# Kernel tuning notes

Hardware: AMD Instinct MI355X
Metric: run time of the kernel (lower is better)

The kernel has to match this reference:

```python
import jax, jax.numpy as jnp
import numpy as np

VOCAB = 30001  # vocab_size + 1
EMB = 64
CHAR = 50
RNN = 128
TAGS = 9
B, T = 256, 512
D_IN = EMB + CHAR  # 114


def lstm_scan(x, Wx, Wh, b):
    # x: [T, B, D]; Keras LSTM gate order i, f, g(c), o; sigmoid/tanh activations.
    Bsz = x.shape[1]
    H = Wh.shape[0]
    def step(carry, xt):
        h, c = carry
        z = xt @ Wx + h @ Wh + b  # [B, 4H]
        i, f, g, o = jnp.split(z, 4, axis=-1)
        c = jax.nn.sigmoid(f) * c + jax.nn.sigmoid(i) * jnp.tanh(g)
        h = jax.nn.sigmoid(o) * jnp.tanh(c)
        return (h, c), h
    init = (jnp.zeros((Bsz, H), x.dtype), jnp.zeros((Bsz, H), x.dtype))
    _, hs = jax.lax.scan(step, init, x)
    return hs  # [T, B, H]


def crf_log_likelihood(logits, labels, lengths, trans):
    # logits: [B,T,K]; labels: [B,T] int; lengths: [B] int; trans: [K,K]
    Bsz, Tlen, K = logits.shape
    mask = (jnp.arange(Tlen)[None, :] < lengths[:, None]).astype(logits.dtype)  # [B,T]
    # gold path score: unary + pairwise transition terms
    unary = jnp.take_along_axis(logits, labels[..., None], axis=-1)[..., 0]  # [B,T]
    unary_score = jnp.sum(unary * mask, axis=1)
    binary = trans[labels[:, :-1], labels[:, 1:]]  # [B,T-1]
    binary_score = jnp.sum(binary * mask[:, 1:], axis=1)
    seq_score = unary_score + binary_score
    # forward algorithm (log-domain scan over time)
    logits_t = jnp.transpose(logits, (1, 0, 2))  # [T,B,K]
    mask_t = jnp.transpose(mask[:, 1:])          # [T-1,B]
    def step(alpha, inp):
        logit_t, m = inp
        new = jax.nn.logsumexp(alpha[:, :, None] + trans[None], axis=1) + logit_t
        alpha = jnp.where(m[:, None] > 0, new, alpha)
        return alpha, None
    alpha, _ = jax.lax.scan(step, logits_t[0], (logits_t[1:], mask_t))
    log_norm = jax.nn.logsumexp(alpha, axis=1)
    log_norm = jnp.where(lengths > 0, log_norm, jnp.zeros_like(log_norm))
    return seq_score - log_norm


def setup_inputs() -> dict:
    key = jax.random.key(0)
    ks = jax.random.split(key, 12)
    inputs = jax.random.randint(ks[0], (B, T), 0, 30000, dtype=jnp.int32)
    char_embeddings = jax.random.normal(ks[1], (B, T, CHAR), dtype=jnp.float32)
    labels = jax.random.randint(ks[2], (B, T), 0, TAGS, dtype=jnp.int32)
    E = 0.1 * jax.random.normal(ks[3], (VOCAB, EMB), dtype=jnp.float32)
    s_in = 1.0 / np.sqrt(D_IN)
    s_h = 1.0 / np.sqrt(RNN)
    Wx_f = s_in * jax.random.normal(ks[4], (D_IN, 4 * RNN), dtype=jnp.float32)
    Wh_f = s_h * jax.random.normal(ks[5], (RNN, 4 * RNN), dtype=jnp.float32)
    b_f = jnp.zeros((4 * RNN,), jnp.float32)
    Wx_b = s_in * jax.random.normal(ks[6], (D_IN, 4 * RNN), dtype=jnp.float32)
    Wh_b = s_h * jax.random.normal(ks[7], (RNN, 4 * RNN), dtype=jnp.float32)
    b_b = jnp.zeros((4 * RNN,), jnp.float32)
    Wd = (1.0 / np.sqrt(2 * RNN)) * jax.random.normal(ks[8], (2 * RNN, TAGS), dtype=jnp.float32)
    bd = jnp.zeros((TAGS,), jnp.float32)
    transition = jax.random.uniform(ks[9], (TAGS, TAGS), dtype=jnp.float32)
    return {"inputs": inputs, "char_embeddings": char_embeddings, "labels": labels,
            "E": E, "Wx_f": Wx_f, "Wh_f": Wh_f, "b_f": b_f,
            "Wx_b": Wx_b, "Wh_b": Wh_b, "b_b": b_b,
            "Wd": Wd, "bd": bd, "transition": transition}


def reference(inputs, char_embeddings, labels, E, Wx_f, Wh_f, b_f, Wx_b, Wh_b, b_b, Wd, bd, transition):
    emb = E[inputs]                                      # [B,T,64]
    x = jnp.concatenate([emb, char_embeddings], axis=2)  # [B,T,114]
    xt = jnp.transpose(x, (1, 0, 2))                     # [T,B,114]
    h_f = lstm_scan(xt, Wx_f, Wh_f, b_f)                 # [T,B,128]
    h_b = lstm_scan(xt[::-1], Wx_b, Wh_b, b_b)[::-1]     # [T,B,128]
    out = jnp.concatenate([h_f, h_b], axis=-1)           # [T,B,256]
    logits = jnp.transpose(out, (1, 0, 2)) @ Wd + bd     # [B,T,9]
    lengths = jnp.sum((labels != 0).astype(jnp.int32), axis=1)
    log_likelihood = crf_log_likelihood(logits, labels, lengths, transition)
    return log_likelihood, transition
```

## Files before the change

kernel.cpp:

```cpp
#include <hip/hip_runtime.h>

#define BB   256
#define TT   512
#define EMBD 64
#define CHARD 50
#define DIN  114
#define RNN  128
#define NG   512
#define TAGS 9

typedef __bf16 bf16x8 __attribute__((ext_vector_type(8)));
typedef float  f32x4  __attribute__((ext_vector_type(4)));
typedef unsigned int uint4v __attribute__((ext_vector_type(4)));
union U8 { bf16x8 v; uint4v u; };

static __device__ __forceinline__ unsigned short f2bf(float f) {
  unsigned int u = __float_as_uint(f);
  unsigned int r = (u + 0x7FFFu + ((u >> 16) & 1u)) >> 16;
  return (unsigned short)r;
}
static __device__ __forceinline__ void gl_lds16(const void* g, void* l) {
  __builtin_amdgcn_global_load_lds(
      (const __attribute__((address_space(1))) unsigned int*)g,
      (__attribute__((address_space(3))) unsigned int*)l, 16, 0, 0);
}
static __device__ __forceinline__ int swz(int u) { return u ^ ((u >> 4) & 7); }

__global__ void k_build_x(const int* __restrict__ inp, const float* __restrict__ ch,
                          const float* __restrict__ E, unsigned short* __restrict__ x) {
  int idx = blockIdx.x * 256 + threadIdx.x;
  int k   = idx & 127;
  int row = idx >> 7;
  float v;
  if (k < EMBD)      v = E[inp[row] * EMBD + k];
  else if (k < DIN)  v = ch[row * CHARD + (k - EMBD)];
  else               v = 0.f;
  x[idx] = f2bf(v);
}

__global__ void k_prep_w(const float* __restrict__ Wx_f, const float* __restrict__ Wh_f,
                         const float* __restrict__ Wx_b, const float* __restrict__ Wh_b,
                         const float* __restrict__ Wd,
                         unsigned short* __restrict__ WxT, unsigned short* __restrict__ WhT,
                         unsigned short* __restrict__ WdT) {
  if (blockIdx.x == 512) {
    for (int i = threadIdx.x; i < 16 * 256; i += 256) {
      int n = i >> 8, k = i & 255;
      WdT[i] = (n < TAGS) ? f2bf(Wd[k * TAGS + n]) : (unsigned short)0;
    }
    return;
  }
  int idx = blockIdx.x * 256 + threadIdx.x;
  int dir = idx >> 16;
  int rem = idx & 65535;
  int n   = rem >> 7;
  int kk  = rem & 127;
  const float* Wx = dir ? Wx_b : Wx_f;
  const float* Wh = dir ? Wh_b : Wh_f;
  WxT[idx] = (kk < DIN) ? f2bf(Wx[kk * NG + n]) : (unsigned short)0;
  WhT[idx] = f2bf(Wh[kk * NG + n]);
}

__global__ void k_lengths(const int* __restrict__ labels, int* __restrict__ lengths) {
  int b = blockIdx.x, lane = threadIdx.x;
  int cnt = 0;
  for (int t = lane; t < TT; t += 64) cnt += (labels[b * TT + t] != 0);
  for (int o = 32; o > 0; o >>= 1) cnt += __shfl_down(cnt, o);
  if (lane == 0) lengths[b] = cnt;
}

__global__ __launch_bounds__(512, 2) void k_zgemm(
    const unsigned short* __restrict__ x, const unsigned short* __restrict__ WxT,
    const float* __restrict__ b_f, const float* __restrict__ b_b,
    unsigned short* __restrict__ zbuf, int s0, int TCH) {
  __shared__ __align__(16) unsigned short xr[16384];

  const int bid = blockIdx.x;
  const int dir = bid / (16 * TCH);
  const int rem = bid % (16 * TCH);
  const int bg  = rem / TCH, tch = rem % TCH;
  const int b0  = bg * 16;
  const int sb  = s0 + tch * 16;

  const int tid = threadIdx.x, w = tid >> 6, l = tid & 63;
  const int lq = l & 15, lg = l >> 4;

  const unsigned short* WxD = WxT + dir * (NG * 128);
  const float* bias = dir ? b_b : b_f;

  bf16x8 wx[4][4];
  float bs[4];
  #pragma unroll
  for (int g = 0; g < 4; ++g) {
    int n = g * RNN + w * 16 + lq;
    bs[g] = bias[n];
    #pragma unroll
    for (int kt = 0; kt < 4; ++kt)
      wx[g][kt] = *reinterpret_cast<const bf16x8*>(WxD + n * 128 + kt * 32 + lg * 8);
  }

  auto stage = [&](int ci) {
    int buf = ci & 1;
    #pragma unroll
    for (int j = 0; j < 2; ++j) {
      int idx = w * 2 + j, sc = idx >> 2, kt = idx & 3;
      int s = sb + ci * 4 + sc;
      int t = dir ? (TT - 1 - s) : s;
      gl_lds16(x + ((size_t)(b0 + lq) * TT + t) * 128 + kt * 32 + lg * 8,
               xr + buf * 8192 + sc * 2048 + kt * 512);
    }
  };

  stage(0);
  for (int ci = 0; ci < 4; ++ci) {
    asm volatile("s_waitcnt vmcnt(0) lgkmcnt(0)" ::: "memory");
    __builtin_amdgcn_s_barrier();
    if (ci < 3) stage(ci + 1);
    int buf = ci & 1;
    #pragma unroll
    for (int sc = 0; sc < 4; ++sc) {
      int s = sb + ci * 4 + sc;
      bf16x8 xf[4];
      #pragma unroll
      for (int kt = 0; kt < 4; ++kt)
        xf[kt] = *reinterpret_cast<const bf16x8*>(xr + buf * 8192 + sc * 2048 + kt * 512 + l * 8);
      f32x4 acc[4];
      #pragma unroll
      for (int g = 0; g < 4; ++g) acc[g] = f32x4{bs[g], bs[g], bs[g], bs[g]};
      #pragma unroll
      for (int kt = 0; kt < 4; ++kt)
        #pragma unroll
        for (int g = 0; g < 4; ++g)
          acc[g] = __builtin_amdgcn_mfma_f32_16x16x32_bf16(xf[kt], wx[g][kt], acc[g], 0, 0, 0);
      U8 zlo, zhi;
      #pragma unroll
      for (int g = 0; g < 2; ++g)
        #pragma unroll
        for (int r = 0; r < 4; ++r) {
          zlo.v[g * 4 + r] = (__bf16)acc[g][r];
          zhi.v[g * 4 + r] = (__bf16)acc[g + 2][r];
        }
      unsigned short* zp = zbuf + (size_t)(s - s0) * 262144 + dir * 131072 +
                           bg * 8192 + w * 1024 + l * 16;
      *reinterpret_cast<bf16x8*>(zp)     = zlo.v;
      *reinterpret_cast<bf16x8*>(zp + 8) = zhi.v;
    }
  }
}

__global__ __launch_bounds__(512, 2) void k_lstm(
    const unsigned short* __restrict__ zbuf, const unsigned short* __restrict__ WhT,
    unsigned short* __restrict__ hseq, float* __restrict__ cbuf,
    int s0, int s1, int first) {
  __shared__ __align__(16) unsigned short hr[16384];

  const int wg = blockIdx.x, dir = wg >> 4, bg = wg & 15, b0 = bg * 16;
  const int tid = threadIdx.x, w = tid >> 6, l = tid & 63;
  const int lq = l & 15, lg = l >> 4;

  const unsigned short* WhD = WhT + dir * (NG * 128);
  unsigned short* hout = hseq + (size_t)dir * ((size_t)BB * TT * 128);
  char* hrb = reinterpret_cast<char*>(hr);

  bf16x8 wh[4][4];
  #pragma unroll
  for (int g = 0; g < 4; ++g) {
    int n = g * RNN + w * 16 + lq;
    #pragma unroll
    for (int kt = 0; kt < 4; ++kt)
      wh[g][kt] = *reinterpret_cast<const bf16x8*>(WhD + n * 128 + kt * 32 + lg * 8);
  }

  int ro[4];
  #pragma unroll
  for (int kt = 0; kt < 4; ++kt) ro[kt] = swz(kt * 64 + l) * 16;
  int wo[4];
  #pragma unroll
  for (int r = 0; r < 4; ++r) {
    int u = (w >> 1) * 64 + ((w & 1) * 2 + (lq >> 3)) * 16 + lg * 4 + r;
    wo[r] = swz(u) * 16 + (lq & 7) * 2;
  }

  f32x4 c;
  if (first) {
    c = f32x4{0.f, 0.f, 0.f, 0.f};
    if (tid < 256) {
      int h16 = tid & 15, row = tid >> 4;
      int u = (h16 >> 2) * 64 + (h16 & 3) * 16 + row;
      *reinterpret_cast<f32x4*>(hrb + 7 * 4096 + swz(u) * 16) = f32x4{0.f, 0.f, 0.f, 0.f};
    }
  } else {
    #pragma unroll
    for (int r = 0; r < 4; ++r)
      c[r] = cbuf[(size_t)(dir * BB + b0 + lg * 4 + r) * RNN + w * 16 + lq];
    if (tid < 256) {
      int h16 = tid & 15, row = tid >> 4;
      int tprev = dir ? (TT - s0) : (s0 - 1);
      bf16x8 v = *reinterpret_cast<const bf16x8*>(
          hout + ((size_t)(b0 + row) * TT + tprev) * 128 + h16 * 8);
      int u = (h16 >> 2) * 64 + (h16 & 3) * 16 + row;
      *reinterpret_cast<bf16x8*>(hrb + 7 * 4096 + swz(u) * 16) = v;
    }
  }
  __syncthreads();

  const unsigned short* zQ = zbuf + dir * 131072 + bg * 8192 + w * 1024 + l * 16;
  bf16x8 zAl = *reinterpret_cast<const bf16x8*>(zQ);
  bf16x8 zAh = *reinterpret_cast<const bf16x8*>(zQ + 8);
  bf16x8 zBl = *reinterpret_cast<const bf16x8*>(zQ + 262144);
  bf16x8 zBh = *reinterpret_cast<const bf16x8*>(zQ + 262144 + 8);

  auto gather = [&](int sp) {
    #pragma unroll
    for (int j = 0; j < 2; ++j) {
      int ut = tid + j * 512;
      int h16 = ut & 15, tc = (ut >> 4) & 3, row = ut >> 6;
      int s = sp + tc;
      int t = dir ? (TT - 1 - s) : s;
      int u = (h16 >> 2) * 64 + (h16 & 3) * 16 + row;
      bf16x8 v = *reinterpret_cast<const bf16x8*>(hrb + (s & 7) * 4096 + swz(u) * 16);
      *reinterpret_cast<bf16x8*>(hout + ((size_t)(b0 + row) * TT + t) * 128 + h16 * 8) = v;
    }
  };

  for (int s = s0; s < s1; ++s) {
    U8 ul, uh; ul.v = zAl; uh.v = zAh;
    f32x4 acc[4];
    acc[0] = f32x4{__uint_as_float(ul.u[0] << 16), __uint_as_float(ul.u[0] & 0xffff0000u),
                   __uint_as_float(ul.u[1] << 16), __uint_as_float(ul.u[1] & 0xffff0000u)};
    acc[1] = f32x4{__uint_as_float(ul.u[2] << 16), __uint_as_float(ul.u[2] & 0xffff0000u),
                   __uint_as_float(ul.u[3] << 16), __uint_as_float(ul.u[3] & 0xffff0000u)};
    acc[2] = f32x4{__uint_as_float(uh.u[0] << 16), __uint_as_float(uh.u[0] & 0xffff0000u),
                   __uint_as_float(uh.u[1] << 16), __uint_as_float(uh.u[1] & 0xffff0000u)};
    acc[3] = f32x4{__uint_as_float(uh.u[2] << 16), __uint_as_float(uh.u[2] & 0xffff0000u),
                   __uint_as_float(uh.u[3] << 16), __uint_as_float(uh.u[3] & 0xffff0000u)};
    zAl = zBl; zAh = zBh;
    int sn = s + 2; if (sn > s1 - 1) sn = s1 - 1;
    const unsigned short* zp = zQ + (size_t)(sn - s0) * 262144;
    zBl = *reinterpret_cast<const bf16x8*>(zp);
    zBh = *reinterpret_cast<const bf16x8*>(zp + 8);

    const char* hb = hrb + ((s - 1) & 7) * 4096;
    bf16x8 hf[4];
    #pragma unroll
    for (int kt = 0; kt < 4; ++kt)
      hf[kt] = *reinterpret_cast<const bf16x8*>(hb + ro[kt]);
    #pragma unroll
    for (int kt = 0; kt < 4; ++kt)
      #pragma unroll
      for (int g = 0; g < 4; ++g)
        acc[g] = __builtin_amdgcn_mfma_f32_16x16x32_bf16(hf[kt], wh[g][kt], acc[g], 0, 0, 0);

    if ((s & 3) == 0 && s > s0) gather(s - 4);

    char* hwslot = hrb + (s & 7) * 4096;
    #pragma unroll
    for (int r = 0; r < 4; ++r) {
      float zi = acc[0][r], zf = acc[1][r], zg = acc[2][r], zo = acc[3][r];
      float si = __builtin_amdgcn_rcpf(1.f + __expf(-zi));
      float sf = __builtin_amdgcn_rcpf(1.f + __expf(-zf));
      float so = __builtin_amdgcn_rcpf(1.f + __expf(-zo));
      float tg = 1.f - 2.f * __builtin_amdgcn_rcpf(__expf(2.f * zg) + 1.f);
      float cn = sf * c[r] + si * tg;
      float th = 1.f - 2.f * __builtin_amdgcn_rcpf(__expf(2.f * cn) + 1.f);
      c[r] = cn;
      *reinterpret_cast<unsigned short*>(hwslot + wo[r]) = f2bf(so * th);
    }
    asm volatile("s_waitcnt lgkmcnt(0)" ::: "memory");
    __builtin_amdgcn_s_barrier();
  }

  gather(s1 - 4);
  #pragma unroll
  for (int r = 0; r < 4; ++r)
    cbuf[(size_t)(dir * BB + b0 + lg * 4 + r) * RNN + w * 16 + lq] = c[r];
}

__global__ __launch_bounds__(256) void k_logits(const unsigned short* __restrict__ hseq,
                                                const unsigned short* __restrict__ WdT,
                                                const float* __restrict__ bd,
                                                float* __restrict__ logits) {
  __shared__ __align__(16) unsigned short xt[2][16384];
  const int tid = threadIdx.x, wv = tid >> 6, l = tid & 63;
  const int lq = l & 15, lg = l >> 4;
  const size_t HS = (size_t)BB * TT * 128;

  bf16x8 wb[8];
  #pragma unroll
  for (int kt = 0; kt < 8; ++kt)
    wb[kt] = *reinterpret_cast<const bf16x8*>(WdT + lq * 256 + kt * 32 + lg * 8);
  float bdv = (lq < TAGS) ? bd[lq] : 0.f;

  auto stage = [&](int it, int buf) {
    int bt0 = blockIdx.x * 256 + it * 64;
    #pragma unroll
    for (int i = 0; i < 8; ++i) {
      int v = tid + i * 256;
      int g = v ^ ((v >> 5) & 7);
      int row = g >> 5, cu = g & 31;
      const unsigned short* src = (cu < 16)
          ? hseq + (size_t)(bt0 + row) * 128 + cu * 8
          : hseq + HS + (size_t)(bt0 + row) * 128 + (cu - 16) * 8;
      gl_lds16(src, &xt[buf][(i * 256 + wv * 64) * 8]);
    }
  };

  stage(0, 0);
  for (int it = 0; it < 4; ++it) {
    asm volatile("s_waitcnt vmcnt(12)" ::: "memory");
    __builtin_amdgcn_s_barrier();
    if (it < 3) stage(it + 1, (it + 1) & 1);
    int buf = it & 1;
    int bt0 = blockIdx.x * 256 + it * 64;
    int r0 = wv * 16;
    bf16x8 af[8];
    #pragma unroll
    for (int kt = 0; kt < 8; ++kt) {
      int u = (r0 + lq) * 32 + kt * 4 + lg;
      af[kt] = *reinterpret_cast<const bf16x8*>(&xt[buf][(u ^ ((u >> 5) & 7)) * 8]);
    }
    f32x4 acc = f32x4{bdv, bdv, bdv, bdv};
    #pragma unroll
    for (int kt = 0; kt < 8; ++kt)
      acc = __builtin_amdgcn_mfma_f32_16x16x32_bf16(af[kt], wb[kt], acc, 0, 0, 0);
    if (lq < TAGS) {
      #pragma unroll
      for (int r = 0; r < 4; ++r)
        logits[(size_t)(bt0 + r0 + lg * 4 + r) * TAGS + lq] = acc[r];
    }
    asm volatile("s_waitcnt lgkmcnt(0)" ::: "memory");
  }
}

__global__ void k_crf(const float* __restrict__ logits, const int* __restrict__ labels,
                      const int* __restrict__ lengths, const float* __restrict__ trans,
                      float* __restrict__ out) {
  int b = blockIdx.x;
  int lane = threadIdx.x;
  int len = lengths[b];
  const float* lg = logits + (size_t)b * TT * TAGS;
  const int*   lab = labels + b * TT;

  float sc = 0.f;
  for (int t = lane; t < TT; t += 64) {
    if (t < len) {
      sc += lg[t * TAGS + lab[t]];
      if (t >= 1) sc += trans[lab[t - 1] * TAGS + lab[t]];
    }
  }
  for (int o = 32; o > 0; o >>= 1) sc += __shfl_down(sc, o);
  sc = __shfl(sc, 0);

  int j = (lane < TAGS) ? lane : 0;
  float Tc[TAGS];
  #pragma unroll
  for (int i = 0; i < TAGS; ++i) Tc[i] = trans[i * TAGS + j];
  float alpha[TAGS];
  #pragma unroll
  for (int i = 0; i < TAGS; ++i) alpha[i] = lg[i];

  float pre[8];
  #pragma unroll
  for (int k = 0; k < 8; ++k) pre[k] = (1 + k < TT) ? lg[(1 + k) * TAGS + j] : 0.f;

  for (int tb = 1; tb < TT; tb += 8) {
    #pragma unroll
    for (int u = 0; u < 8; ++u) {
      int t = tb + u;
      if (t < TT) {
        float m = -1e30f;
        #pragma unroll
        for (int i = 0; i < TAGS; ++i) m = fmaxf(m, alpha[i] + Tc[i]);
        float ssum = 0.f;
        #pragma unroll
        for (int i = 0; i < TAGS; ++i) ssum += __expf(alpha[i] + Tc[i] - m);
        float nj = m + __logf(ssum) + pre[u];
        int tf = t + 8;
        pre[u] = (tf < TT) ? lg[tf * TAGS + j] : 0.f;
        bool upd = (t < len);
        float na[TAGS];
        #pragma unroll
        for (int i = 0; i < TAGS; ++i) na[i] = __shfl(nj, i);
        if (upd)
          #pragma unroll
          for (int i = 0; i < TAGS; ++i) alpha[i] = na[i];
      }
    }
  }
  if (lane == 0) {
    float m = -1e30f;
    #pragma unroll
    for (int i = 0; i < TAGS; ++i) m = fmaxf(m, alpha[i]);
    float ssum = 0.f;
    #pragma unroll
    for (int i = 0; i < TAGS; ++i) ssum += __expf(alpha[i] - m);
    float ln = m + __logf(ssum);
    out[b] = (len > 0) ? (sc - ln) : 0.f;
  }
}

__global__ void k_copy_trans(const float* __restrict__ trans, float* __restrict__ out) {
  int i = threadIdx.x;
  if (i < TAGS * TAGS) out[BB + i] = trans[i];
}

extern "C" void kernel_launch(void* const* d_in, const int* in_sizes, int n_in,
                              void* d_out, int out_size, void* d_ws, size_t ws_size,
                              hipStream_t stream) {
  const int*   inp    = (const int*)d_in[0];
  const float* ch     = (const float*)d_in[1];
  const int*   labels = (const int*)d_in[2];
  const float* E      = (const float*)d_in[3];
  const float* Wx_f   = (const float*)d_in[4];
  const float* Wh_f   = (const float*)d_in[5];
  const float* b_f    = (const float*)d_in[6];
  const float* Wx_b   = (const float*)d_in[7];
  const float* Wh_b   = (const float*)d_in[8];
  const float* b_b    = (const float*)d_in[9];
  const float* Wd     = (const float*)d_in[10];
  const float* bd     = (const float*)d_in[11];
  const float* trans  = (const float*)d_in[12];
  float* out = (float*)d_out;

  unsigned short* x    = (unsigned short*)d_ws;
  unsigned short* hseq = x + (size_t)BB * TT * 128;
  unsigned short* WxT  = hseq + (size_t)2 * BB * TT * 128;
  unsigned short* WhT  = WxT + 2 * NG * 128;
  unsigned short* WdT  = WhT + 2 * NG * 128;
  float* logits        = (float*)(WdT + 16 * 256);
  float* cbuf          = logits + (size_t)BB * TT * TAGS;
  int*   lengths       = (int*)(cbuf + (size_t)2 * BB * RNN);
  unsigned short* zbuf = (unsigned short*)(lengths + 256);

  const size_t fixed_b = 106439680ull;
  int NP = 32;
  const int cands[5] = {2, 4, 8, 16, 32};
  for (int i = 0; i < 5; ++i) {
    if (fixed_b + (size_t)(TT / cands[i]) * 524288ull <= ws_size) { NP = cands[i]; break; }
  }
  const int L = TT / NP;

  k_build_x<<<(BB * TT * 128) / 256, 256, 0, stream>>>(inp, ch, E, x);
  k_prep_w<<<513, 256, 0, stream>>>(Wx_f, Wh_f, Wx_b, Wh_b, Wd, WxT, WhT, WdT);
  k_lengths<<<BB, 64, 0, stream>>>(labels, lengths);
  for (int p = 0; p < NP; ++p) {
    int s0 = p * L;
    k_zgemm<<<2 * 16 * (L / 16), 512, 0, stream>>>(x, WxT, b_f, b_b, zbuf, s0, L / 16);
    k_lstm<<<32, 512, 0, stream>>>(zbuf, WhT, hseq, cbuf, s0, s0 + L, p == 0);
  }
  k_logits<<<(BB * TT) / 256, 256, 0, stream>>>(hseq, WdT, bd, logits);
  k_crf<<<BB, 64, 0, stream>>>(logits, labels, lengths, trans, out);
  k_copy_trans<<<1, 128, 0, stream>>>(trans, out);
}
```

Baseline: 748.2 us.

## Fuse input-projection GEMM and LSTM recurrence into one pipelined kernel

Merges the z-GEMM and LSTM kernels into a single launch. Recurrence blocks handle chunk p while extra blocks compute the input projections for chunk p+1 into a double-buffered fp32 z buffer, so the two phases overlap. LSTM blocks now cover 8 batch rows with 256 threads across 64 workgroups instead of 16 rows with 512 threads across 32, which exposes more parallelism in the serial time loop. Gate math is restructured to use fewer reciprocals, with clamping and a permlane32 swap to redistribute accumulators. z is stored in fp32 rather than bf16, which doubles z traffic and workspace, and the chunk count is now chosen from fewer options based on workspace size.

After: 930.1 us. +24.3%, slower.

```diff
diff --git a/kernel.cpp b/kernel.cpp
--- a/kernel.cpp
+++ b/kernel.cpp
@@ -11,8 +11,6 @@
 
 typedef __bf16 bf16x8 __attribute__((ext_vector_type(8)));
 typedef float  f32x4  __attribute__((ext_vector_type(4)));
-typedef unsigned int uint4v __attribute__((ext_vector_type(4)));
-union U8 { bf16x8 v; uint4v u; };
 
 static __device__ __forceinline__ unsigned short f2bf(float f) {
   unsigned int u = __float_as_uint(f);
@@ -24,7 +22,6 @@
       (const __attribute__((address_space(1))) unsigned int*)g,
       (__attribute__((address_space(3))) unsigned int*)l, 16, 0, 0);
 }
-static __device__ __forceinline__ int swz(int u) { return u ^ ((u >> 4) & 7); }
 
 __global__ void k_build_x(const int* __restrict__ inp, const float* __restrict__ ch,
                           const float* __restrict__ E, unsigned short* __restrict__ x) {
@@ -69,211 +66,245 @@
   if (lane == 0) lengths[b] = cnt;
 }
 
-__global__ __launch_bounds__(512, 2) void k_zgemm(
-    const unsigned short* __restrict__ x, const unsigned short* __restrict__ WxT,
+__global__ __launch_bounds__(256, 1) void k_fused(
+    const unsigned short* __restrict__ x,
+    const unsigned short* __restrict__ WxT,
+    const unsigned short* __restrict__ WhT,
     const float* __restrict__ b_f, const float* __restrict__ b_b,
-    unsigned short* __restrict__ zbuf, int s0, int TCH) {
-  __shared__ __align__(16) unsigned short xr[16384];
-
-  const int bid = blockIdx.x;
-  const int dir = bid / (16 * TCH);
-  const int rem = bid % (16 * TCH);
-  const int bg  = rem / TCH, tch = rem % TCH;
-  const int b0  = bg * 16;
-  const int sb  = s0 + tch * 16;
-
+    const float* __restrict__ zcons, float* __restrict__ zprod,
+    unsigned short* __restrict__ hseq, float* __restrict__ cbuf,
+    int lstm_n, int s0, int s1, int first, int zs0, int znsteps)
+{
+  __shared__ __align__(16) char LDS[32768];
   const int tid = threadIdx.x, w = tid >> 6, l = tid & 63;
   const int lq = l & 15, lg = l >> 4;
 
-  const unsigned short* WxD = WxT + dir * (NG * 128);
-  const float* bias = dir ? b_b : b_f;
-
-  bf16x8 wx[4][4];
-  float bs[4];
-  #pragma unroll
-  for (int g = 0; g < 4; ++g) {
-    int n = g * RNN + w * 16 + lq;
-    bs[g] = bias[n];
+  if ((int)blockIdx.x < lstm_n) {
+    const int wg = blockIdx.x, dir = wg >> 5, rg = wg & 31, b0 = rg * 8;
+    const unsigned short* WhD = WhT + dir * (NG * 128);
+    unsigned short* hout = hseq + (size_t)dir * ((size_t)BB * TT * 128);
+    char* ring = LDS;
+
+    bf16x8 wh[4][2][4];
+    #pragma unroll
+    for (int g = 0; g < 4; ++g)
+      #pragma unroll
+      for (int j = 0; j < 2; ++j) {
+        int n = g * RNN + w * 32 + j * 16 + lq;
+        #pragma unroll
+        for (int kt = 0; kt < 4; ++kt)
+          wh[g][j][kt] = *reinterpret_cast<const bf16x8*>(WhD + n * 128 + kt * 32 + lg * 8);
+      }
+
+    const int hidden = w * 32 + (lg >> 1) * 16 + lq;
+    const int ku  = hidden >> 3;
+    const int inb = (hidden & 7) * 2;
+    const int row7 = l & 7;
+    int ro[4];
     #pragma unroll
     for (int kt = 0; kt < 4; ++kt)
-      wx[g][kt] = *reinterpret_cast<const bf16x8*>(WxD + n * 128 + kt * 32 + lg * 8);
-  }
-
-  auto stage = [&](int ci) {
-    int buf = ci & 1;
-    #pragma unroll
-    for (int j = 0; j < 2; ++j) {
-      int idx = w * 2 + j, sc = idx >> 2, kt = idx & 3;
-      int s = sb + ci * 4 + sc;
-      int t = dir ? (TT - 1 - s) : s;
-      gl_lds16(x + ((size_t)(b0 + lq) * TT + t) * 128 + kt * 32 + lg * 8,
-               xr + buf * 8192 + sc * 2048 + kt * 512);
-    }
-  };
-
-  stage(0);
-  for (int ci = 0; ci < 4; ++ci) {
-    asm volatile("s_waitcnt vmcnt(0) lgkmcnt(0)" ::: "memory");
-    __builtin_amdgcn_s_barrier();
-    if (ci < 3) stage(ci + 1);
-    int buf = ci & 1;
-    #pragma unroll
-    for (int sc = 0; sc < 4; ++sc) {
-      int s = sb + ci * 4 + sc;
-      bf16x8 xf[4];
+      ro[kt] = (row7 * 16 + (((kt * 4) + lg) ^ row7)) * 16;
+
+    if (tid < 128) {
+      int row = tid >> 4, h16 = tid & 15;
+      int unit = row * 16 + (h16 ^ row);
+      if (first) {
+        *reinterpret_cast<f32x4*>(ring + 7 * 2048 + unit * 16) = f32x4{0.f, 0.f, 0.f, 0.f};
+      } else {
+        int tprev = dir ? (TT - s0) : (s0 - 1);
+        bf16x8 v = *reinterpret_cast<const bf16x8*>(
+            hout + ((size_t)(b0 + row) * TT + tprev) * 128 + h16 * 8);
+        *reinterpret_cast<bf16x8*>(ring + 7 * 2048 + unit * 16) = v;
+      }
+    }
+    float c[4];
+    #pragma unroll
+    for (int r = 0; r < 4; ++r) {
+      int rowc = (lg & 1) * 4 + r;
+      c[r] = first ? 0.f : cbuf[(size_t)(dir * BB + b0 + rowc) * RNN + hidden];
+    }
+    __syncthreads();
+
+    const float* zrec = zcons + ((size_t)((dir * 32 + rg) * 4 + w)) * 1024 + (lg * 16 + lq) * 32;
+    f32x4 zc[8];
+    if (lg < 2) {
+      #pragma unroll
+      for (int i = 0; i < 8; ++i) zc[i] = *reinterpret_cast<const f32x4*>(zrec + i * 4);
+    }
+
+    for (int s = s0; s < s1; ++s) {
+      f32x4 acc[4][2];
+      #pragma unroll
+      for (int g = 0; g < 4; ++g)
+        #pragma unroll
+        for (int j = 0; j < 2; ++j)
+          acc[g][j] = (lg < 2) ? zc[g * 2 + j] : f32x4{0.f, 0.f, 0.f, 0.f};
+      {
+        int sn = (s + 1 < s1) ? (s + 1) : (s1 - 1);
+        if (lg < 2) {
+          const float* zp = zrec + (size_t)(sn - s0) * 262144;
+          #pragma unroll
+          for (int i = 0; i < 8; ++i) zc[i] = *reinterpret_cast<const f32x4*>(zp + i * 4);
+        }
+      }
+
+      const char* rb = ring + ((s - 1) & 7) * 2048;
+      bf16x8 hf[4];
       #pragma unroll
       for (int kt = 0; kt < 4; ++kt)
-        xf[kt] = *reinterpret_cast<const bf16x8*>(xr + buf * 8192 + sc * 2048 + kt * 512 + l * 8);
-      f32x4 acc[4];
-      #pragma unroll
-      for (int g = 0; g < 4; ++g) acc[g] = f32x4{bs[g], bs[g], bs[g], bs[g]};
+        hf[kt] = *reinterpret_cast<const bf16x8*>(rb + ro[kt]);
       #pragma unroll
       for (int kt = 0; kt < 4; ++kt)
         #pragma unroll
+        for (int g = 0; g < 4; ++g) {
+          acc[g][0] = __builtin_amdgcn_mfma_f32_16x16x32_bf16(hf[kt], wh[g][0][kt], acc[g][0], 0, 0, 0);
+          acc[g][1] = __builtin_amdgcn_mfma_f32_16x16x32_bf16(hf[kt], wh[g][1][kt], acc[g][1], 0, 0, 0);
+        }
+
+      if ((s & 3) == 0 && s > s0) {
+        int sp = s - 4;
+        #pragma unroll
+        for (int j = 0; j < 2; ++j) {
+          int u = tid + j * 256;
+          int h16 = u & 15, tc = (u >> 4) & 3, row = u >> 6;
+          int ss = sp + tc, t = dir ? (TT - 1 - ss) : ss;
+          bf16x8 v = *reinterpret_cast<const bf16x8*>(
+              ring + (ss & 7) * 2048 + (row * 16 + (h16 ^ row)) * 16);
+          *reinterpret_cast<bf16x8*>(hout + ((size_t)(b0 + row) * TT + t) * 128 + h16 * 8) = v;
+        }
+      }
+
+      float sw[4][4];
+      #pragma unroll
+      for (int g = 0; g < 4; ++g)
+        #pragma unroll
+        for (int r = 0; r < 4; ++r) {
+          float d = acc[g][1][r], srcv = acc[g][1][r];
+          asm volatile("v_permlane32_swap_b32 %0, %1" : "+v"(d), "+v"(srcv));
+          sw[g][r] = d;
+        }
+
+      char* ws_ = ring + (s & 7) * 2048;
+      #pragma unroll
+      for (int r = 0; r < 4; ++r) {
+        float zi = (lg < 2) ? acc[0][0][r] : sw[0][r];
+        float zf = (lg < 2) ? acc[1][0][r] : sw[1][r];
+        float zg = (lg < 2) ? acc[2][0][r] : sw[2][r];
+        float zo = (lg < 2) ? acc[3][0][r] : sw[3][r];
+        zi = fminf(20.f, fmaxf(-20.f, zi));
+        zf = fminf(20.f, fmaxf(-20.f, zf));
+        zg = fminf(20.f, fmaxf(-20.f, zg));
+        zo = fminf(20.f, fmaxf(-20.f, zo));
+        float ei = __expf(-zi), ef = __expf(-zf), eo = __expf(-zo);
+        float g2 = __expf(2.f * zg);
+        float P   = (1.f + ei) * (g2 + 1.f);
+        float efp = 1.f + ef;
+        float num = c[r] * P + efp * (g2 - 1.f);
+        float cn  = num * __builtin_amdgcn_rcpf(efp * P);
+        c[r] = cn;
+        float cc = fminf(20.f, fmaxf(-20.f, cn));
+        float ec = __expf(2.f * cc);
+        float hn = (ec - 1.f) * __builtin_amdgcn_rcpf((1.f + eo) * (ec + 1.f));
+        int rowr = (lg & 1) * 4 + r;
+        int unit = rowr * 16 + (ku ^ rowr);
+        *reinterpret_cast<unsigned short*>(ws_ + unit * 16 + inb) = f2bf(hn);
+      }
+      __syncthreads();
+    }
+
+    {
+      int sp = s1 - 4;
+      #pragma unroll
+      for (int j = 0; j < 2; ++j) {
+        int u = tid + j * 256;
+        int h16 = u & 15, tc = (u >> 4) & 3, row = u >> 6;
+        int ss = sp + tc, t = dir ? (TT - 1 - ss) : ss;
+        bf16x8 v = *reinterpret_cast<const bf16x8*>(
+            ring + (ss & 7) * 2048 + (row * 16 + (h16 ^ row)) * 16);
+        *reinterpret_cast<bf16x8*>(hout + ((size_t)(b0 + row) * TT + t) * 128 + h16 * 8) = v;
+      }
+    }
+    #pragma unroll
+    for (int r = 0; r < 4; ++r) {
+      int rowc = (lg & 1) * 4 + r;
+      cbuf[(size_t)(dir * BB + b0 + rowc) * RNN + hidden] = c[r];
+    }
+  } else {
+    if (znsteps <= 0) return;
+    const int TCHN = znsteps >> 4;
+    const int zb = blockIdx.x - lstm_n;
+    const int per = 16 * TCHN;
+    const int dir = zb / per;
+    const int rem = zb % per;
+    const int rg2 = rem / TCHN, tch = rem % TCHN;
+    const int b0p = rg2 * 16;
+    const int sb  = zs0 + tch * 16;
+
+    const unsigned short* WxD = WxT + dir * (NG * 128);
+    const float* bias = dir ? b_b : b_f;
+    unsigned short* xr = (unsigned short*)LDS;
+
+    bf16x8 wx[4][2][4];
+    float  bs[4][2];
+    #pragma unroll
+    for (int g = 0; g < 4; ++g)
+      #pragma unroll
+      for (int j = 0; j < 2; ++j) {
+        int n = g * RNN + w * 32 + j * 16 + lq;
+        bs[g][j] = bias[n];
+        #pragma unroll
+        for (int kt = 0; kt < 4; ++kt)
+          wx[g][j][kt] = *reinterpret_cast<const bf16x8*>(WxD + n * 128 + kt * 32 + lg * 8);
+      }
+
+    auto stage = [&](int ci) {
+      int buf = ci & 1;
+      #pragma unroll
+      for (int jj = 0; jj < 4; ++jj) {
+        int idx = w * 4 + jj, sc = idx >> 2, kt = idx & 3;
+        int s = sb + ci * 4 + sc;
+        int t = dir ? (TT - 1 - s) : s;
+        gl_lds16(x + ((size_t)(b0p + lq) * TT + t) * 128 + kt * 32 + lg * 8,
+                 xr + buf * 8192 + sc * 2048 + kt * 512);
+      }
+    };
+
+    stage(0);
+    for (int ci = 0; ci < 4; ++ci) {
+      __syncthreads();
+      if (ci < 3) stage(ci + 1);
+      int buf = ci & 1;
+      #pragma unroll
+      for (int sc = 0; sc < 4; ++sc) {
+        int s = sb + ci * 4 + sc;
+        bf16x8 xf[4];
+        #pragma unroll
+        for (int kt = 0; kt < 4; ++kt)
+          xf[kt] = *reinterpret_cast<const bf16x8*>(xr + buf * 8192 + sc * 2048 + kt * 512 + l * 8);
+        f32x4 acc[4][2];
+        #pragma unroll
         for (int g = 0; g < 4; ++g)
-          acc[g] = __builtin_amdgcn_mfma_f32_16x16x32_bf16(xf[kt], wx[g][kt], acc[g], 0, 0, 0);
-      U8 zlo, zhi;
-      #pragma unroll
-      for (int g = 0; g < 2; ++g)
-        #pragma unroll
-        for (int r = 0; r < 4; ++r) {
-          zlo.v[g * 4 + r] = (__bf16)acc[g][r];
-          zhi.v[g * 4 + r] = (__bf16)acc[g + 2][r];
-        }
-      unsigned short* zp = zbuf + (size_t)(s - s0) * 262144 + dir * 131072 +
-                           bg * 8192 + w * 1024 + l * 16;
-      *reinterpret_cast<bf16x8*>(zp)     = zlo.v;
-      *reinterpret_cast<bf16x8*>(zp + 8) = zhi.v;
-    }
-  }
-}
-
-__global__ __launch_bounds__(512, 2) void k_lstm(
-    const unsigned short* __restrict__ zbuf, const unsigned short* __restrict__ WhT,
-    unsigned short* __restrict__ hseq, float* __restrict__ cbuf,
-    int s0, int s1, int first) {
-  __shared__ __align__(16) unsigned short hr[16384];
-
-  const int wg = blockIdx.x, dir = wg >> 4, bg = wg & 15, b0 = bg * 16;
-  const int tid = threadIdx.x, w = tid >> 6, l = tid & 63;
-  const int lq = l & 15, lg = l >> 4;
-
-  const unsigned short* WhD = WhT + dir * (NG * 128);
-  unsigned short* hout = hseq + (size_t)dir * ((size_t)BB * TT * 128);
-  char* hrb = reinterpret_cast<char*>(hr);
-
-  bf16x8 wh[4][4];
-  #pragma unroll
-  for (int g = 0; g < 4; ++g) {
-    int n = g * RNN + w * 16 + lq;
-    #pragma unroll
-    for (int kt = 0; kt < 4; ++kt)
-      wh[g][kt] = *reinterpret_cast<const bf16x8*>(WhD + n * 128 + kt * 32 + lg * 8);
-  }
-
-  int ro[4];
-  #pragma unroll
-  for (int kt = 0; kt < 4; ++kt) ro[kt] = swz(kt * 64 + l) * 16;
-  int wo[4];
-  #pragma unroll
-  for (int r = 0; r < 4; ++r) {
-    int u = (w >> 1) * 64 + ((w & 1) * 2 + (lq >> 3)) * 16 + lg * 4 + r;
-    wo[r] = swz(u) * 16 + (lq & 7) * 2;
-  }
-
-  f32x4 c;
-  if (first) {
-    c = f32x4{0.f, 0.f, 0.f, 0.f};
-    if (tid < 256) {
-      int h16 = tid & 15, row = tid >> 4;
-      int u = (h16 >> 2) * 64 + (h16 & 3) * 16 + row;
-      *reinterpret_cast<f32x4*>(hrb + 7 * 4096 + swz(u) * 16) = f32x4{0.f, 0.f, 0.f, 0.f};
-    }
-  } else {
-    #pragma unroll
-    for (int r = 0; r < 4; ++r)
-      c[r] = cbuf[(size_t)(dir * BB + b0 + lg * 4 + r) * RNN + w * 16 + lq];
-    if (tid < 256) {
-      int h16 = tid & 15, row = tid >> 4;
-      int tprev = dir ? (TT - s0) : (s0 - 1);
-      bf16x8 v = *reinterpret_cast<const bf16x8*>(
-          hout + ((size_t)(b0 + row) * TT + tprev) * 128 + h16 * 8);
-      int u = (h16 >> 2) * 64 + (h16 & 3) * 16 + row;
-      *reinterpret_cast<bf16x8*>(hrb + 7 * 4096 + swz(u) * 16) = v;
-    }
-  }
-  __syncthreads();
-
-  const unsigned short* zQ = zbuf + dir * 131072 + bg * 8192 + w * 1024 + l * 16;
-  bf16x8 zAl = *reinterpret_cast<const bf16x8*>(zQ);
-  bf16x8 zAh = *reinterpret_cast<const bf16x8*>(zQ + 8);
-  bf16x8 zBl = *reinterpret_cast<const bf16x8*>(zQ + 262144);
-  bf16x8 zBh = *reinterpret_cast<const bf16x8*>(zQ + 262144 + 8);
-
-  auto gather = [&](int sp) {
-    #pragma unroll
-    for (int j = 0; j < 2; ++j) {
-      int ut = tid + j * 512;
-      int h16 = ut & 15, tc = (ut >> 4) & 3, row = ut >> 6;
-      int s = sp + tc;
-      int t = dir ? (TT - 1 - s) : s;
-      int u = (h16 >> 2) * 64 + (h16 & 3) * 16 + row;
-      bf16x8 v = *reinterpret_cast<const bf16x8*>(hrb + (s & 7) * 4096 + swz(u) * 16);
-      *reinterpret_cast<bf16x8*>(hout + ((size_t)(b0 + row) * TT + t) * 128 + h16 * 8) = v;
-    }
-  };
-
-  for (int s = s0; s < s1; ++s) {
-    U8 ul, uh; ul.v = zAl; uh.v = zAh;
-    f32x4 acc[4];
-    acc[0] = f32x4{__uint_as_float(ul.u[0] << 16), __uint_as_float(ul.u[0] & 0xffff0000u),
-                   __uint_as_float(ul.u[1] << 16), __uint_as_float(ul.u[1] & 0xffff0000u)};
-    acc[1] = f32x4{__uint_as_float(ul.u[2] << 16), __uint_as_float(ul.u[2] & 0xffff0000u),
-                   __uint_as_float(ul.u[3] << 16), __uint_as_float(ul.u[3] & 0xffff0000u)};
-    acc[2] = f32x4{__uint_as_float(uh.u[0] << 16), __uint_as_float(uh.u[0] & 0xffff0000u),
-                   __uint_as_float(uh.u[1] << 16), __uint_as_float(uh.u[1] & 0xffff0000u)};
-    acc[3] = f32x4{__uint_as_float(uh.u[2] << 16), __uint_as_float(uh.u[2] & 0xffff0000u),
-                   __uint_as_float(uh.u[3] << 16), __uint_as_float(uh.u[3] & 0xffff0000u)};
-    zAl = zBl; zAh = zBh;
-    int sn = s + 2; if (sn > s1 - 1) sn = s1 - 1;
-    const unsigned short* zp = zQ + (size_t)(sn - s0) * 262144;
-    zBl = *reinterpret_cast<const bf16x8*>(zp);
-    zBh = *reinterpret_cast<const bf16x8*>(zp + 8);
-
-    const char* hb = hrb + ((s - 1) & 7) * 4096;
-    bf16x8 hf[4];
-    #pragma unroll
-    for (int kt = 0; kt < 4; ++kt)
-      hf[kt] = *reinterpret_cast<const bf16x8*>(hb + ro[kt]);
-    #pragma unroll
-    for (int kt = 0; kt < 4; ++kt)
-      #pragma unroll
-      for (int g = 0; g < 4; ++g)
-        acc[g] = __builtin_amdgcn_mfma_f32_16x16x32_bf16(hf[kt], wh[g][kt], acc[g], 0, 0, 0);
-
-    if ((s & 3) == 0 && s > s0) gather(s - 4);
-
-    char* hwslot = hrb + (s & 7) * 4096;
-    #pragma unroll
-    for (int r = 0; r < 4; ++r) {
-      float zi = acc[0][r], zf = acc[1][r], zg = acc[2][r], zo = acc[3][r];
-      float si = __builtin_amdgcn_rcpf(1.f + __expf(-zi));
-      float sf = __builtin_amdgcn_rcpf(1.f + __expf(-zf));
-      float so = __builtin_amdgcn_rcpf(1.f + __expf(-zo));
-      float tg = 1.f - 2.f * __builtin_amdgcn_rcpf(__expf(2.f * zg) + 1.f);
-      float cn = sf * c[r] + si * tg;
-      float th = 1.f - 2.f * __builtin_amdgcn_rcpf(__expf(2.f * cn) + 1.f);
-      c[r] = cn;
-      *reinterpret_cast<unsigned short*>(hwslot + wo[r]) = f2bf(so * th);
-    }
-    asm volatile("s_waitcnt lgkmcnt(0)" ::: "memory");
-    __builtin_amdgcn_s_barrier();
-  }
-
-  gather(s1 - 4);
-  #pragma unroll
-  for (int r = 0; r < 4; ++r)
-    cbuf[(size_t)(dir * BB + b0 + lg * 4 + r) * RNN + w * 16 + lq] = c[r];
+          #pragma unroll
+          for (int j = 0; j < 2; ++j)
+            acc[g][j] = f32x4{bs[g][j], bs[g][j], bs[g][j], bs[g][j]};
+        #pragma unroll
+        for (int kt = 0; kt < 4; ++kt)
+          #pragma unroll
+          for (int g = 0; g < 4; ++g) {
+            acc[g][0] = __builtin_amdgcn_mfma_f32_16x16x32_bf16(xf[kt], wx[g][0][kt], acc[g][0], 0, 0, 0);
+            acc[g][1] = __builtin_amdgcn_mfma_f32_16x16x32_bf16(xf[kt], wx[g][1][kt], acc[g][1], 0, 0, 0);
+          }
+        float* zp = zprod + (size_t)(s - zs0) * 262144 +
+                    ((size_t)((dir * 32 + rg2 * 2 + (lg >> 1)) * 4 + w)) * 1024 +
+                    ((lg & 1) * 16 + lq) * 32;
+        #pragma unroll
+        for (int g = 0; g < 4; ++g)
+          #pragma unroll
+          for (int j = 0; j < 2; ++j)
+            *reinterpret_cast<f32x4*>(zp + g * 8 + j * 4) = acc[g][j];
+      }
+    }
+  }
 }
 
 __global__ __launch_bounds__(256) void k_logits(const unsigned short* __restrict__ hseq,
@@ -307,8 +338,7 @@
 
   stage(0, 0);
   for (int it = 0; it < 4; ++it) {
-    asm volatile("s_waitcnt vmcnt(12)" ::: "memory");
-    __builtin_amdgcn_s_barrier();
+    __syncthreads();
     if (it < 3) stage(it + 1, (it + 1) & 1);
     int buf = it & 1;
     int bt0 = blockIdx.x * 256 + it * 64;
@@ -328,7 +358,6 @@
       for (int r = 0; r < 4; ++r)
         logits[(size_t)(bt0 + r0 + lg * 4 + r) * TAGS + lq] = acc[r];
     }
-    asm volatile("s_waitcnt lgkmcnt(0)" ::: "memory");
   }
 }
 
@@ -430,24 +459,32 @@
   float* logits        = (float*)(WdT + 16 * 256);
   float* cbuf          = logits + (size_t)BB * TT * TAGS;
   int*   lengths       = (int*)(cbuf + (size_t)2 * BB * RNN);
-  unsigned short* zbuf = (unsigned short*)(lengths + 256);
+  float* zbuf          = (float*)(lengths + 256);
 
   const size_t fixed_b = 106439680ull;
-  int NP = 32;
-  const int cands[5] = {2, 4, 8, 16, 32};
-  for (int i = 0; i < 5; ++i) {
-    if (fixed_b + (size_t)(TT / cands[i]) * 524288ull <= ws_size) { NP = cands[i]; break; }
-  }
+  int NP = 8;
+  if (fixed_b + 2ull * (TT / 8)  * 1048576ull > ws_size) NP = 16;
+  if (fixed_b + 2ull * (TT / 16) * 1048576ull > ws_size) NP = 32;
   const int L = TT / NP;
+  const size_t zsl = (size_t)L * 262144;
 
   k_build_x<<<(BB * TT * 128) / 256, 256, 0, stream>>>(inp, ch, E, x);
   k_prep_w<<<513, 256, 0, stream>>>(Wx_f, Wh_f, Wx_b, Wh_b, Wd, WxT, WhT, WdT);
   k_lengths<<<BB, 64, 0, stream>>>(labels, lengths);
+
+  k_fused<<<2 * L, 256, 0, stream>>>(x, WxT, WhT, b_f, b_b,
+                                     zbuf, zbuf, hseq, cbuf,
+                                     0, 0, 0, 1, 0, L);
   for (int p = 0; p < NP; ++p) {
-    int s0 = p * L;
-    k_zgemm<<<2 * 16 * (L / 16), 512, 0, stream>>>(x, WxT, b_f, b_b, zbuf, s0, L / 16);
-    k_lstm<<<32, 512, 0, stream>>>(zbuf, WhT, hseq, cbuf, s0, s0 + L, p == 0);
-  }
+    int nz = (p + 1 < NP) ? 2 * L : 0;
+    k_fused<<<64 + nz, 256, 0, stream>>>(
+        x, WxT, WhT, b_f, b_b,
+        zbuf + (size_t)(p & 1) * zsl,
+        zbuf + (size_t)((p + 1) & 1) * zsl,
+        hseq, cbuf,
+        64, p * L, (p + 1) * L, (p == 0) ? 1 : 0, (p + 1) * L, nz ? L : 0);
+  }
+
   k_logits<<<(BB * TT) / 256, 256, 0, stream>>>(hseq, WdT, bd, logits);
   k_crf<<<BB, 64, 0, stream>>>(logits, labels, lengths, trans, out);
   k_copy_trans<<<1, 128, 0, stream>>>(trans, out);
```
